# Kernel optimization log

Hardware: AMD Instinct MI355X
Metric: run time of the kernel (lower is better)

The kernel has to match this reference:

```python
import jax, jax.numpy as jnp
import numpy as np

B, T, N, F, D, E = 8, 256, 118, 3, 128, 372
G = B * T  # number of graphs after flattening batch*time


def _gcn(x, src, dst, W, b):
    # x: [G, N, Fin] -> PyG GCNConv: X' = D^-1/2 (A+I) D^-1/2 (X W) + b
    h = x @ W  # [G, N, Fout]
    deg = jnp.ones((N,), h.dtype).at[dst].add(1.0)  # in-degree + self loop
    inv = deg ** -0.5
    norm = inv[src] * inv[dst]  # [E]
    agg = h * (1.0 / deg)[None, :, None]  # self-loop term: inv[i]*inv[i] = 1/deg
    agg = agg.at[:, dst].add(h[:, src] * norm[None, :, None])
    return agg + b


def _lstm_layer(x, Wih, Whh, bih, bhh):
    # x: [B, T, I]; PyTorch gate order i, f, g, o
    Bb, H = x.shape[0], Whh.shape[1]
    h0 = jnp.zeros((Bb, H), x.dtype)
    c0 = jnp.zeros((Bb, H), x.dtype)

    def step(carry, xt):
        h, c = carry
        gates = xt @ Wih.T + h @ Whh.T + bih + bhh
        i, f, g, o = jnp.split(gates, 4, axis=-1)
        c = jax.nn.sigmoid(f) * c + jax.nn.sigmoid(i) * jnp.tanh(g)
        h = jax.nn.sigmoid(o) * jnp.tanh(c)
        return (h, c), h

    _, ys = jax.lax.scan(step, (h0, c0), jnp.swapaxes(x, 0, 1))
    return jnp.swapaxes(ys, 0, 1)


def setup_inputs() -> dict:
    key = jax.random.key(0)
    ks = jax.random.split(key, 24)
    s = 0.05

    def rn(i, shape):
        return jax.random.normal(ks[i], shape, jnp.float32) * s

    return {
        "snapshot_sequence": jax.random.normal(ks[0], (B, T, N, F), jnp.float32),
        "edge_index": jax.random.randint(ks[1], (2, E), 0, N, dtype=jnp.int64),
        "scale": jnp.ones((F,), jnp.float32),
        "shift": jnp.zeros((F,), jnp.float32),
        "W1": rn(2, (F, D)), "b1": jnp.zeros((D,), jnp.float32),
        "W2": rn(3, (D, D)), "b2": jnp.zeros((D,), jnp.float32),
        "W3": rn(4, (D, D)), "b3": jnp.zeros((D,), jnp.float32),
        "Wih0": rn(5, (4 * D, D)), "Whh0": rn(6, (4 * D, D)),
        "bih0": jnp.zeros((4 * D,), jnp.float32), "bhh0": jnp.zeros((4 * D,), jnp.float32),
        "Wih1": rn(7, (4 * D, D)), "Whh1": rn(8, (4 * D, D)),
        "bih1": jnp.zeros((4 * D,), jnp.float32), "bhh1": jnp.zeros((4 * D,), jnp.float32),
        "hW1": rn(9, (D, 128)), "hb1": jnp.zeros((128,), jnp.float32),
        "hW2": rn(10, (128, 64)), "hb2": jnp.zeros((64,), jnp.float32),
        "hW3": rn(11, (64, 2)), "hb3": jnp.zeros((2,), jnp.float32),
    }


def reference(snapshot_sequence, edge_index, scale, shift,
              W1, b1, W2, b2, W3, b3,
              Wih0, Whh0, bih0, bhh0, Wih1, Whh1, bih1, bhh1,
              hW1, hb1, hW2, hb2, hW3, hb3):
    src, dst = edge_index[0], edge_index[1]
    x = snapshot_sequence * scale + shift              # FeatureNormalizer
    x = x.reshape(G, N, F)                             # flatten batch*time graphs
    x = jax.nn.silu(_gcn(x, src, dst, W1, b1))         # GCNConv 1 (dropout = eval identity)
    x = jax.nn.silu(_gcn(x, src, dst, W2, b2))         # GCNConv 2
    x = jax.nn.silu(_gcn(x, src, dst, W3, b3))         # GCNConv 3
    emb = x.mean(axis=1)                               # global_mean_pool -> [G, D]
    emb = emb.reshape(B, T, D)
    h = _lstm_layer(emb, Wih0, Whh0, bih0, bhh0)       # 2-layer LSTM (eval: no dropout)
    h = _lstm_layer(h, Wih1, Whh1, bih1, bhh1)
    final = h[:, -1, :]                                # [B, D]
    y = jax.nn.silu(final @ hW1 + hb1)
    y = jax.nn.silu(y @ hW2 + hb2)
    y = y @ hW3 + hb3
    return jax.nn.softplus(y) + 1e-6                   # [B, 2]
```

## Files before the change

kernel.cpp:

```cpp
#include <hip/hip_runtime.h>
#include <math.h>

#define NN 118
#define EE 372
#define GG 2048
#define DD 128
#define TT 256
#define BB 8
#define FD 512

#define XS 136

typedef short bf16x8 __attribute__((ext_vector_type(8)));
typedef float f32x4  __attribute__((ext_vector_type(4)));
typedef _Float16 f16x2 __attribute__((ext_vector_type(2)));

__device__ __forceinline__ float frcp_(float x) { return __builtin_amdgcn_rcpf(x); }
__device__ __forceinline__ float sig_f(float x) { return frcp_(1.0f + __expf(-x)); }
__device__ __forceinline__ float tanh_f(float x) { return 1.0f - 2.0f * frcp_(__expf(2.0f * x) + 1.0f); }
__device__ __forceinline__ float silu_f(float x) { return x * frcp_(1.0f + __expf(-x)); }
__device__ __forceinline__ float siluf_(float x) { return x / (1.0f + expf(-x)); }

__device__ __forceinline__ float fdot2_(unsigned int a, unsigned int b, float c) {
#if defined(__has_builtin) && __has_builtin(__builtin_amdgcn_fdot2)
    return __builtin_amdgcn_fdot2(__builtin_bit_cast(f16x2, a),
                                  __builtin_bit_cast(f16x2, b), c, false);
#else
    f16x2 x = __builtin_bit_cast(f16x2, a), y = __builtin_bit_cast(f16x2, b);
    return c + (float)x[0] * (float)y[0] + (float)x[1] * (float)y[1];
#endif
}

__device__ __forceinline__ void bar_lds() {
    asm volatile("s_waitcnt lgkmcnt(0)\n\ts_barrier" ::: "memory");
}

__device__ __forceinline__ unsigned short f2bf(float x) {
    unsigned int u = __float_as_uint(x);
    unsigned int r = (u + 0x7fffu + ((u >> 16) & 1u)) >> 16;
    return (unsigned short)r;
}
__device__ __forceinline__ float bf2f(unsigned short b) {
    return __uint_as_float(((unsigned int)b) << 16);
}

__global__ void prep_kernel(const int* __restrict__ ei,
                            const float* __restrict__ bih0, const float* __restrict__ bhh0,
                            const float* __restrict__ bih1, const float* __restrict__ bhh1,
                            float* __restrict__ bias0, float* __restrict__ bias1,
                            unsigned short* __restrict__ AbG) {
    __shared__ int sflag;
    __shared__ int ssrc[EE], sdst[EE];
    __shared__ int scount[NN];
    __shared__ float sinv[NN];
    __shared__ float Adense[NN * NN];
    int tid = threadIdx.x;
    if (tid == 0) sflag = 0;
    __syncthreads();
    for (int i = tid; i < 2 * EE; i += blockDim.x)
        if ((i & 1) && ei[i] != 0) atomicOr(&sflag, 1);
    __syncthreads();
    bool m64 = (sflag == 0);
    for (int e = tid; e < EE; e += blockDim.x) {
        int s, d;
        if (m64) { s = ei[2 * e]; d = ei[2 * EE + 2 * e]; }
        else     { s = ei[e];     d = ei[EE + e]; }
        s = min(max(s, 0), NN - 1); d = min(max(d, 0), NN - 1);
        ssrc[e] = s; sdst[e] = d;
    }
    for (int n = tid; n < NN; n += blockDim.x) scount[n] = 0;
    for (int i = tid; i < NN * NN; i += blockDim.x) Adense[i] = 0.0f;
    __syncthreads();
    for (int e = tid; e < EE; e += blockDim.x) atomicAdd(&scount[sdst[e]], 1);
    __syncthreads();
    for (int n = tid; n < NN; n += blockDim.x) {
        float deg = 1.0f + (float)scount[n];
        sinv[n] = rsqrtf(deg);
        Adense[n * NN + n] = 1.0f / deg;
    }
    __syncthreads();
    for (int e = tid; e < EE; e += blockDim.x)
        atomicAdd(&Adense[sdst[e] * NN + ssrc[e]], sinv[ssrc[e]] * sinv[sdst[e]]);
    __syncthreads();
    for (int i = tid; i < 128 * 128; i += blockDim.x) {
        int r = i >> 7, c = i & 127;
        AbG[i] = (r < NN && c < NN) ? f2bf(Adense[r * NN + c]) : (unsigned short)0;
    }
    for (int j = tid; j < FD; j += blockDim.x) {
        bias0[j] = bih0[j] + bhh0[j];
        bias1[j] = bih1[j] + bhh1[j];
    }
}

__global__ void convw_kernel(const float* __restrict__ W, unsigned short* __restrict__ out) {
    int i = blockIdx.x * 512 + threadIdx.x;
    int n = i >> 7, k = i & 127;
    out[i] = f2bf(W[k * DD + n]);
}

__global__ void convh_kernel(const float* __restrict__ W, unsigned int* __restrict__ out) {
    int i = blockIdx.x * 512 + threadIdx.x;
    float a = W[2 * i], b = W[2 * i + 1];
    unsigned short lo = __builtin_bit_cast(unsigned short, (_Float16)a);
    unsigned short hi = __builtin_bit_cast(unsigned short, (_Float16)b);
    out[i] = (unsigned int)lo | ((unsigned int)hi << 16);
}

__global__ void transpose_kernel(const float* __restrict__ in, float* __restrict__ out) {
    int idx = blockIdx.x * blockDim.x + threadIdx.x;
    int j = idx >> 7, k = idx & 127;
    out[k * FD + j] = in[idx];
}

__device__ __forceinline__ void load_m(const unsigned short* __restrict__ src,
                                       unsigned short* __restrict__ dst, int tid) {
    const uint4* s4 = (const uint4*)src;
    for (int c = tid; c < 2048; c += 512) {
        int r = c >> 4, k8 = (c & 15) * 8;
        uint4 v = s4[c];
        *(uint4*)(dst + r * XS + k8) = v;
    }
}

__device__ __forceinline__ void mm_xw(const unsigned short* __restrict__ xb,
                                      const unsigned short* __restrict__ wt,
                                      unsigned short* __restrict__ hS, int tid) {
    int lane = tid & 63, w = tid >> 6;
    int lm = lane & 15, lq = lane >> 4;
    int wm = (w & 1) * 64, wn = (w >> 1) * 32;
    f32x4 acc[4][2];
#pragma unroll
    for (int mt = 0; mt < 4; ++mt)
#pragma unroll
        for (int nt = 0; nt < 2; ++nt) acc[mt][nt] = (f32x4){0.f, 0.f, 0.f, 0.f};
#pragma unroll
    for (int kb = 0; kb < 4; ++kb) {
        int ko = kb * 32 + lq * 8;
        bf16x8 b0 = *(const bf16x8*)(wt + (wn + lm) * XS + ko);
        bf16x8 b1 = *(const bf16x8*)(wt + (wn + 16 + lm) * XS + ko);
#pragma unroll
        for (int mt = 0; mt < 4; ++mt) {
            bf16x8 af = *(const bf16x8*)(xb + (wm + mt * 16 + lm) * XS + ko);
            acc[mt][0] = __builtin_amdgcn_mfma_f32_16x16x32_bf16(af, b0, acc[mt][0], 0, 0, 0);
            acc[mt][1] = __builtin_amdgcn_mfma_f32_16x16x32_bf16(af, b1, acc[mt][1], 0, 0, 0);
        }
    }
#pragma unroll
    for (int mt = 0; mt < 4; ++mt)
#pragma unroll
        for (int nt = 0; nt < 2; ++nt) {
            f32x4 a = acc[mt][nt];
            ushort4 pk;
            pk.x = f2bf(a[0]); pk.y = f2bf(a[1]); pk.z = f2bf(a[2]); pk.w = f2bf(a[3]);
            *(ushort4*)(hS + (wn + nt * 16 + lm) * XS + wm + mt * 16 + lq * 4) = pk;
        }
}

__device__ __forceinline__ void mm_agg(const unsigned short* __restrict__ Ab,
                                       const unsigned short* __restrict__ hS,
                                       unsigned short* __restrict__ xb,
                                       float bn0, float bn1, int tid) {
    int lane = tid & 63, w = tid >> 6;
    int lm = lane & 15, lq = lane >> 4;
    int wm = (w & 1) * 64, wn = (w >> 1) * 32;
    f32x4 acc[4][2];
#pragma unroll
    for (int mt = 0; mt < 4; ++mt)
#pragma unroll
        for (int nt = 0; nt < 2; ++nt) acc[mt][nt] = (f32x4){0.f, 0.f, 0.f, 0.f};
#pragma unroll
    for (int kb = 0; kb < 4; ++kb) {
        int ko = kb * 32 + lq * 8;
        bf16x8 b0 = *(const bf16x8*)(hS + (wn + lm) * XS + ko);
        bf16x8 b1 = *(const bf16x8*)(hS + (wn + 16 + lm) * XS + ko);
#pragma unroll
        for (int mt = 0; mt < 4; ++mt) {
            bf16x8 af = *(const bf16x8*)(Ab + (wm + mt * 16 + lm) * XS + ko);
            acc[mt][0] = __builtin_amdgcn_mfma_f32_16x16x32_bf16(af, b0, acc[mt][0], 0, 0, 0);
            acc[mt][1] = __builtin_amdgcn_mfma_f32_16x16x32_bf16(af, b1, acc[mt][1], 0, 0, 0);
        }
    }
#pragma unroll
    for (int mt = 0; mt < 4; ++mt)
#pragma unroll
        for (int nt = 0; nt < 2; ++nt) {
            float bn = nt ? bn1 : bn0;
            int col = wn + nt * 16 + lm;
#pragma unroll
            for (int i = 0; i < 4; ++i) {
                float v = silu_f(acc[mt][nt][i] + bn);
                xb[(wm + mt * 16 + lq * 4 + i) * XS + col] = f2bf(v);
            }
        }
}

__global__ __launch_bounds__(512) void gcn_kernel(
    const float* __restrict__ xg, const float* __restrict__ scale, const float* __restrict__ shift,
    const float* __restrict__ W1, const float* __restrict__ b1,
    const float* __restrict__ b2, const float* __restrict__ b3,
    const unsigned short* __restrict__ AbG,
    const unsigned short* __restrict__ Wt2g, const unsigned short* __restrict__ Wt3g,
    float* __restrict__ emb) {
    extern __shared__ char smem[];
    unsigned short* xb = (unsigned short*)smem;
    unsigned short* hS = (unsigned short*)(smem + 34816);
    unsigned short* Ab = (unsigned short*)(smem + 69632);
    unsigned short* wt = (unsigned short*)(smem + 104448);
    float* xinL  = (float*)(smem + 139264);
    float* meanS = (float*)(smem + 140688);
    int tid = threadIdx.x;
    int lane = tid & 63, w = tid >> 6;
    int g = blockIdx.x;

    for (int i = tid; i < 2176; i += 512) ((uint4*)hS)[i] = (uint4){0, 0, 0, 0};
    for (int i = tid; i < 170; i += 512) ((uint4*)(xb + NN * XS))[i] = (uint4){0, 0, 0, 0};
    float s0 = scale[0], s1 = scale[1], s2 = scale[2];
    float t0 = shift[0], t1 = shift[1], t2 = shift[2];
    const float* xrow = xg + (size_t)g * (NN * 3);
    for (int i = tid; i < NN * 3; i += 512) {
        int f = i % 3;
        float sc = (f == 0) ? s0 : ((f == 1) ? s1 : s2);
        float sf = (f == 0) ? t0 : ((f == 1) ? t1 : t2);
        xinL[i] = xrow[i] * sc + sf;
    }
    load_m(AbG, Ab, tid);
    load_m(Wt2g, wt, tid);
    int lm = lane & 15;
    int wn = (w >> 1) * 32;
    int n0 = wn + lm, n1 = wn + 16 + lm;
    float b1a = b1[n0], b1b = b1[n1];
    float b2a = b2[n0], b2b = b2[n1];
    float b3a = b3[n0], b3b = b3[n1];
    int dd = lane * 2;
    float2 w10 = *(const float2*)(W1 + dd);
    float2 w11 = *(const float2*)(W1 + DD + dd);
    float2 w12 = *(const float2*)(W1 + 2 * DD + dd);
    bar_lds();
    for (int k = 0; k < 15; ++k) {
        int n = w + 8 * k;
        if (n >= NN) break;
        float x0 = xinL[n * 3], x1 = xinL[n * 3 + 1], x2 = xinL[n * 3 + 2];
        hS[dd * XS + n]       = f2bf(x0 * w10.x + x1 * w11.x + x2 * w12.x);
        hS[(dd + 1) * XS + n] = f2bf(x0 * w10.y + x1 * w11.y + x2 * w12.y);
    }
    bar_lds();
    mm_agg(Ab, hS, xb, b1a, b1b, tid);
    bar_lds();
    mm_xw(xb, wt, hS, tid);
    bar_lds();
    load_m(Wt3g, wt, tid);
    mm_agg(Ab, hS, xb, b2a, b2b, tid);
    bar_lds();
    mm_xw(xb, wt, hS, tid);
    bar_lds();
    mm_agg(Ab, hS, xb, b3a, b3b, tid);
    bar_lds();
    {
        int d = tid & 127, part = tid >> 7;
        int a0 = part * 30;
        int a1 = (a0 + 30 < NN) ? (a0 + 30) : NN;
        float s = 0.f;
        for (int n = a0; n < a1; ++n) s += bf2f(xb[n * XS + d]);
        meanS[part * 128 + d] = s;
    }
    bar_lds();
    if (tid < 128) {
        float s = meanS[tid] + meanS[128 + tid] + meanS[256 + tid] + meanS[384 + tid];
        emb[(size_t)g * DD + tid] = s * (1.0f / (float)NN);
    }
}

__global__ __launch_bounds__(512) void proj_kernel(const float* __restrict__ src,
                                                   const float* __restrict__ WT,
                                                   const float* __restrict__ bias,
                                                   float* __restrict__ dst) {
    __shared__ __align__(16) float eL[DD];
    int g = blockIdx.x, tid = threadIdx.x;
    if (tid < DD) eL[tid] = src[(size_t)g * DD + tid];
    __syncthreads();
    float acc = bias[tid];
    const float* wt = WT + tid;
#pragma unroll 8
    for (int k = 0; k < DD; ++k) acc += eL[k] * wt[(size_t)k * FD];
    dst[(size_t)g * FD + tid] = acc;
}

__global__ __launch_bounds__(512) void scan_kernel(const float* __restrict__ inp,
                                                   const unsigned int* __restrict__ Wh16,
                                                   float* __restrict__ hout, int full) {
    __shared__ __align__(16) unsigned int sh2[64];
    __shared__ float sg[FD];
    int b = blockIdx.x, j = threadIdx.x;
    uint4 wreg[16];
    const uint4* wp = ((const uint4*)Wh16) + (size_t)j * 16;
#pragma unroll
    for (int q = 0; q < 16; ++q) wreg[q] = wp[q];
    float creg = 0.f;
    if (j < 64) sh2[j] = 0u;
    bar_lds();
    const float* ib = inp + (size_t)b * TT * FD;
    float* hb_ = hout + (size_t)b * (full ? TT * DD : DD);
    bool isg = (j >= 2 * DD) && (j < 3 * DD);
    int d = j & 127;
    float g0 = ib[j];
    float g1 = ib[FD + j];
    float g2 = ib[2 * FD + j];
    for (int t = 0; t < TT; ++t) {
        float g3 = (t + 3 < TT) ? ib[(t + 3) * FD + j] : 0.f;
        const uint4* h4 = (const uint4*)sh2;
        float acc = g0;
#pragma unroll
        for (int q = 0; q < 16; ++q) {
            uint4 hv = h4[q];
            uint4 wv = wreg[q];
            acc = fdot2_(wv.x, hv.x, acc);
            acc = fdot2_(wv.y, hv.y, acc);
            acc = fdot2_(wv.z, hv.z, acc);
            acc = fdot2_(wv.w, hv.w, acc);
        }
        sg[j] = isg ? tanh_f(acc) : sig_f(acc);
        bar_lds();
        float iv = sg[d], fv = sg[DD + d], gv = sg[2 * DD + d], ov = sg[3 * DD + d];
        float cn = fv * creg + iv * gv;
        creg = cn;
        float hn = ov * tanh_f(cn);
        if (j < DD) {
            ((_Float16*)sh2)[j] = (_Float16)hn;
            if (full) hb_[t * DD + j] = hn;
            else if (t == TT - 1) hb_[j] = hn;
        }
        bar_lds();
        g0 = g1; g1 = g2; g2 = g3;
    }
}

__global__ void head_kernel(const float* __restrict__ hfin,
                            const float* __restrict__ hW1, const float* __restrict__ hb1,
                            const float* __restrict__ hW2, const float* __restrict__ hb2,
                            const float* __restrict__ hW3, const float* __restrict__ hb3,
                            float* __restrict__ out) {
    __shared__ float fh[BB * DD];
    __shared__ float y1[BB * DD];
    __shared__ float y2[BB * 64];
    int tid = threadIdx.x;
    for (int i = tid; i < BB * DD; i += 256) fh[i] = hfin[i];
    __syncthreads();
    for (int i = tid; i < BB * DD; i += 256) {
        int bb = i >> 7, jj = i & 127;
        float acc = hb1[jj];
        for (int k = 0; k < DD; ++k) acc += fh[(bb << 7) + k] * hW1[(k << 7) + jj];
        y1[i] = siluf_(acc);
    }
    __syncthreads();
    for (int i = tid; i < BB * 64; i += 256) {
        int bb = i >> 6, jj = i & 63;
        float acc = hb2[jj];
        for (int k = 0; k < DD; ++k) acc += y1[(bb << 7) + k] * hW2[(k << 6) + jj];
        y2[i] = siluf_(acc);
    }
    __syncthreads();
    if (tid < BB * 2) {
        int bb = tid >> 1, m = tid & 1;
        float acc = hb3[m];
        for (int k = 0; k < 64; ++k) acc += y2[(bb << 6) + k] * hW3[k * 2 + m];
        float sp = fmaxf(acc, 0.f) + log1pf(expf(-fabsf(acc)));
        out[tid] = sp + 1e-6f;
    }
}

extern "C" void kernel_launch(void* const* d_in, const int* in_sizes, int n_in,
                              void* d_out, int out_size, void* d_ws, size_t ws_size,
                              hipStream_t stream) {
    const float* snap  = (const float*)d_in[0];
    const int*   edges = (const int*)d_in[1];
    const float* scale = (const float*)d_in[2];
    const float* shift = (const float*)d_in[3];
    const float* W1 = (const float*)d_in[4];
    const float* b1 = (const float*)d_in[5];
    const float* W2 = (const float*)d_in[6];
    const float* b2 = (const float*)d_in[7];
    const float* W3 = (const float*)d_in[8];
    const float* b3 = (const float*)d_in[9];
    const float* Wih0 = (const float*)d_in[10];
    const float* Whh0 = (const float*)d_in[11];
    const float* bih0 = (const float*)d_in[12];
    const float* bhh0 = (const float*)d_in[13];
    const float* Wih1 = (const float*)d_in[14];
    const float* Whh1 = (const float*)d_in[15];
    const float* bih1 = (const float*)d_in[16];
    const float* bhh1 = (const float*)d_in[17];
    const float* hW1 = (const float*)d_in[18];
    const float* hb1 = (const float*)d_in[19];
    const float* hW2 = (const float*)d_in[20];
    const float* hb2 = (const float*)d_in[21];
    const float* hW3 = (const float*)d_in[22];
    const float* hb3 = (const float*)d_in[23];

    float* ws = (float*)d_ws;
    float* bias0 = ws + 0;
    float* bias1 = ws + 512;
    unsigned short* AbG  = (unsigned short*)(ws + 1024);
    unsigned short* Wt2g = (unsigned short*)(ws + 9216);
    unsigned short* Wt3g = (unsigned short*)(ws + 17408);
    float* WT0 = ws + 25600;
    float* WT1 = ws + 91136;
    unsigned int* Wh16_0 = (unsigned int*)(ws + 156672);
    unsigned int* Wh16_1 = (unsigned int*)(ws + 189440);
    float* emb   = ws + 222208;
    float* inp   = ws + 484352;
    float* h0seq = ws + 1532928;
    float* hfin  = ws + 1795072;

    const int smem_gcn = 142736;
    hipFuncSetAttribute((const void*)gcn_kernel,
                        hipFuncAttributeMaxDynamicSharedMemorySize, smem_gcn);

    prep_kernel<<<1, 256, 0, stream>>>(edges, bih0, bhh0, bih1, bhh1,
                                       bias0, bias1, AbG);
    convw_kernel<<<32, 512, 0, stream>>>(W2, Wt2g);
    convw_kernel<<<32, 512, 0, stream>>>(W3, Wt3g);
    convh_kernel<<<64, 512, 0, stream>>>(Whh0, Wh16_0);
    convh_kernel<<<64, 512, 0, stream>>>(Whh1, Wh16_1);
    transpose_kernel<<<128, 512, 0, stream>>>(Wih0, WT0);
    transpose_kernel<<<128, 512, 0, stream>>>(Wih1, WT1);
    gcn_kernel<<<GG, 512, smem_gcn, stream>>>(snap, scale, shift, W1, b1, b2, b3,
                                              AbG, Wt2g, Wt3g, emb);
    proj_kernel<<<GG, 512, 0, stream>>>(emb, WT0, bias0, inp);
    scan_kernel<<<BB, 512, 0, stream>>>(inp, Wh16_0, h0seq, 1);
    proj_kernel<<<GG, 512, 0, stream>>>(h0seq, WT1, bias1, inp);
    scan_kernel<<<BB, 512, 0, stream>>>(inp, Wh16_1, hfin, 0);
    head_kernel<<<1, 256, 0, stream>>>(hfin, hW1, hb1, hW2, hb2, hW3, hb3, (float*)d_out);
}
```

Before: 609.7 us.

## Compute all four LSTM gates per thread with 128-thread scan blocks

The recurrent scan now assigns one hidden unit per thread, which computes all four gate dot products from 256 register-resident fp16 weight pairs. This removes the shared-memory gate exchange and one barrier per timestep, and double-buffers the hidden state. The weight conversion kernel is rewritten to emit a gate/column-interleaved layout for coalesced register loading. The trade-off is 4x serial FMA work per thread, only two waves per block, and heavy register pressure that could spill.

```diff
diff --git a/kernel.cpp b/kernel.cpp
--- a/kernel.cpp
+++ b/kernel.cpp
@@ -100,7 +100,9 @@
 
 __global__ void convh_kernel(const float* __restrict__ W, unsigned int* __restrict__ out) {
     int i = blockIdx.x * 512 + threadIdx.x;
-    float a = W[2 * i], b = W[2 * i + 1];
+    int d = i & 127, q = (i >> 7) & 63, g = i >> 13;
+    const float* row = W + (size_t)(g * 128 + d) * 128;
+    float a = row[2 * q], b = row[2 * q + 1];
     unsigned short lo = __builtin_bit_cast(unsigned short, (_Float16)a);
     unsigned short hi = __builtin_bit_cast(unsigned short, (_Float16)b);
     out[i] = (unsigned int)lo | ((unsigned int)hi << 16);
@@ -285,52 +287,69 @@
     dst[(size_t)g * FD + tid] = acc;
 }
 
-__global__ __launch_bounds__(512) void scan_kernel(const float* __restrict__ inp,
-                                                   const unsigned int* __restrict__ Wh16,
-                                                   float* __restrict__ hout, int full) {
-    __shared__ __align__(16) unsigned int sh2[64];
-    __shared__ float sg[FD];
+__global__ __launch_bounds__(128, 1) void scan_kernel(
+    const float* __restrict__ inp,
+    const unsigned int* __restrict__ Wc,
+    float* __restrict__ hout, int full) {
+    __shared__ __align__(16) unsigned short hL[2][DD];
     int b = blockIdx.x, j = threadIdx.x;
-    uint4 wreg[16];
-    const uint4* wp = ((const uint4*)Wh16) + (size_t)j * 16;
-#pragma unroll
-    for (int q = 0; q < 16; ++q) wreg[q] = wp[q];
+    unsigned int wreg[4][64];
+#pragma unroll
+    for (int g = 0; g < 4; ++g)
+#pragma unroll
+        for (int q = 0; q < 64; ++q)
+            wreg[g][q] = Wc[(g * 64 + q) * 128 + j];
+#pragma unroll
+    for (int g = 0; g < 4; ++g)
+#pragma unroll
+        for (int q = 0; q < 64; ++q)
+            asm volatile("" : "+v"(wreg[g][q]));
+    hL[0][j] = 0; hL[1][j] = 0;
     float creg = 0.f;
-    if (j < 64) sh2[j] = 0u;
-    bar_lds();
     const float* ib = inp + (size_t)b * TT * FD;
     float* hb_ = hout + (size_t)b * (full ? TT * DD : DD);
-    bool isg = (j >= 2 * DD) && (j < 3 * DD);
-    int d = j & 127;
-    float g0 = ib[j];
-    float g1 = ib[FD + j];
-    float g2 = ib[2 * FD + j];
+    float xg0[4], xg1[4];
+#pragma unroll
+    for (int g = 0; g < 4; ++g) { xg0[g] = ib[g * DD + j]; xg1[g] = ib[FD + g * DD + j]; }
+    bar_lds();
     for (int t = 0; t < TT; ++t) {
-        float g3 = (t + 3 < TT) ? ib[(t + 3) * FD + j] : 0.f;
-        const uint4* h4 = (const uint4*)sh2;
-        float acc = g0;
-#pragma unroll
-        for (int q = 0; q < 16; ++q) {
-            uint4 hv = h4[q];
-            uint4 wv = wreg[q];
-            acc = fdot2_(wv.x, hv.x, acc);
-            acc = fdot2_(wv.y, hv.y, acc);
-            acc = fdot2_(wv.z, hv.z, acc);
-            acc = fdot2_(wv.w, hv.w, acc);
+        float xg2[4];
+        bool more = (t + 2 < TT);
+#pragma unroll
+        for (int g = 0; g < 4; ++g)
+            xg2[g] = more ? ib[(t + 2) * FD + g * DD + j] : 0.f;
+        const uint4* h4 = (const uint4*)hL[t & 1];
+        float a0 = xg0[0], a1 = xg0[1], a2 = xg0[2], a3 = xg0[3];
+#pragma unroll
+        for (int c = 0; c < 16; ++c) {
+            uint4 hv = h4[c];
+            a0 = fdot2_(wreg[0][4 * c + 0], hv.x, a0);
+            a1 = fdot2_(wreg[1][4 * c + 0], hv.x, a1);
+            a2 = fdot2_(wreg[2][4 * c + 0], hv.x, a2);
+            a3 = fdot2_(wreg[3][4 * c + 0], hv.x, a3);
+            a0 = fdot2_(wreg[0][4 * c + 1], hv.y, a0);
+            a1 = fdot2_(wreg[1][4 * c + 1], hv.y, a1);
+            a2 = fdot2_(wreg[2][4 * c + 1], hv.y, a2);
+            a3 = fdot2_(wreg[3][4 * c + 1], hv.y, a3);
+            a0 = fdot2_(wreg[0][4 * c + 2], hv.z, a0);
+            a1 = fdot2_(wreg[1][4 * c + 2], hv.z, a1);
+            a2 = fdot2_(wreg[2][4 * c + 2], hv.z, a2);
+            a3 = fdot2_(wreg[3][4 * c + 2], hv.z, a3);
+            a0 = fdot2_(wreg[0][4 * c + 3], hv.w, a0);
+            a1 = fdot2_(wreg[1][4 * c + 3], hv.w, a1);
+            a2 = fdot2_(wreg[2][4 * c + 3], hv.w, a2);
+            a3 = fdot2_(wreg[3][4 * c + 3], hv.w, a3);
         }
-        sg[j] = isg ? tanh_f(acc) : sig_f(acc);
-        bar_lds();
-        float iv = sg[d], fv = sg[DD + d], gv = sg[2 * DD + d], ov = sg[3 * DD + d];
+        float iv = sig_f(a0), fv = sig_f(a1), gv = tanh_f(a2), ov = sig_f(a3);
         float cn = fv * creg + iv * gv;
         creg = cn;
         float hn = ov * tanh_f(cn);
-        if (j < DD) {
-            ((_Float16*)sh2)[j] = (_Float16)hn;
-            if (full) hb_[t * DD + j] = hn;
-            else if (t == TT - 1) hb_[j] = hn;
-        }
+        ((_Float16*)hL[(t + 1) & 1])[j] = (_Float16)hn;
+        if (full) hb_[t * DD + j] = hn;
+        else if (t == TT - 1) hb_[j] = hn;
+#pragma unroll
+        for (int g = 0; g < 4; ++g) { xg0[g] = xg1[g]; xg1[g] = xg2[g]; }
         bar_lds();
-        g0 = g1; g1 = g2; g2 = g3;
     }
 }
 
@@ -404,8 +423,8 @@
     unsigned short* Wt3g = (unsigned short*)(ws + 17408);
     float* WT0 = ws + 25600;
     float* WT1 = ws + 91136;
-    unsigned int* Wh16_0 = (unsigned int*)(ws + 156672);
-    unsigned int* Wh16_1 = (unsigned int*)(ws + 189440);
+    unsigned int* Wc0 = (unsigned int*)(ws + 156672);
+    unsigned int* Wc1 = (unsigned int*)(ws + 189440);
     float* emb   = ws + 222208;
     float* inp   = ws + 484352;
     float* h0seq = ws + 1532928;
@@ -419,15 +438,15 @@
                                        bias0, bias1, AbG);
     convw_kernel<<<32, 512, 0, stream>>>(W2, Wt2g);
     convw_kernel<<<32, 512, 0, stream>>>(W3, Wt3g);
-    convh_kernel<<<64, 512, 0, stream>>>(Whh0, Wh16_0);
-    convh_kernel<<<64, 512, 0, stream>>>(Whh1, Wh16_1);
+    convh_kernel<<<64, 512, 0, stream>>>(Whh0, Wc0);
+    convh_kernel<<<64, 512, 0, stream>>>(Whh1, Wc1);
     transpose_kernel<<<128, 512, 0, stream>>>(Wih0, WT0);
     transpose_kernel<<<128, 512, 0, stream>>>(Wih1, WT1);
     gcn_kernel<<<GG, 512, smem_gcn, stream>>>(snap, scale, shift, W1, b1, b2, b3,
                                               AbG, Wt2g, Wt3g, emb);
     proj_kernel<<<GG, 512, 0, stream>>>(emb, WT0, bias0, inp);
-    scan_kernel<<<BB, 512, 0, stream>>>(inp, Wh16_0, h0seq, 1);
+    scan_kernel<<<BB, 128, 0, stream>>>(inp, Wc0, h0seq, 1);
     proj_kernel<<<GG, 512, 0, stream>>>(h0seq, WT1, bias1, inp);
-    scan_kernel<<<BB, 512, 0, stream>>>(inp, Wh16_1, hfin, 0);
+    scan_kernel<<<BB, 128, 0, stream>>>(inp, Wc1, hfin, 0);
     head_kernel<<<1, 256, 0, stream>>>(hfin, hW1, hb1, hW2, hb2, hW3, hb3, (float*)d_out);
 }
```

New measurement: 944.0 us. 54.8% more time.
